# Optimization experiments

Measured on AMD Instinct MI355X. Metric: run time of the kernel, lower is better.

Reference implementation:

```python
import jax, jax.numpy as jnp
import numpy as np

B, S, D = 2, 2048, 1024
H, DH = 16, 64  # num_heads, per-head depth (kd//H == vd//H)
NEG = -1e10


def setup_inputs() -> dict:
    key = jax.random.key(0)
    ks = jax.random.split(key, 5)
    scale = 0.02
    return {
        "X": jax.random.normal(ks[0], (B, S, D), dtype=jnp.float32),
        "Wq": jax.random.normal(ks[1], (D, D), dtype=jnp.float32) * scale,
        "Wk": jax.random.normal(ks[2], (D, D), dtype=jnp.float32) * scale,
        "Wv": jax.random.normal(ks[3], (D, D), dtype=jnp.float32) * scale,
        "Wo": jax.random.normal(ks[4], (D, D), dtype=jnp.float32) * scale,
    }


def reference(X, Wq, Wk, Wv, Wo):
    # torch nn.Linear(in,out,bias=False): y = x @ W.T, W is [out,in]
    q = X @ Wq.T  # [B,S,H*DH]
    k = X @ Wk.T
    v = X @ Wv.T
    # split heads -> [B,H,S,DH]
    q = q.reshape(B, S, H, DH).transpose(0, 2, 1, 3) * (DH ** -0.5)
    k = k.reshape(B, S, H, DH).transpose(0, 2, 1, 3)
    v = v.reshape(B, S, H, DH).transpose(0, 2, 1, 3)
    # causal bias: -1e10 on strictly upper triangle (psuedolikelihood=False)
    bias = NEG * jnp.triu(jnp.ones((S, S), dtype=jnp.float32), 1)
    # logits[...,q,k] = q . k
    logits = jnp.einsum("bhkd,bhqd->bhqk", k, q) + bias
    weights = jax.nn.softmax(logits, axis=-1)  # [B,H,S,S]
    out = jnp.einsum("bhqk,bhkd->bhqd", weights, v)
    out = out.transpose(0, 2, 1, 3).reshape(B, S, H * DH)
    return out @ Wo.T  # [B,S,D]
```

## Files before the change

### kernel.cpp

```cpp
#include <hip/hip_runtime.h>
#include <math.h>


typedef _Float16 f16x8 __attribute__((ext_vector_type(8)));
typedef _Float16 f16x4 __attribute__((ext_vector_type(4)));
typedef _Float16 f16x2 __attribute__((ext_vector_type(2)));
typedef __attribute__((ext_vector_type(4))) float f32x4;
typedef __attribute__((ext_vector_type(16))) float f32x16;

#define MFMA16(a, b, c) __builtin_amdgcn_mfma_f32_16x16x32_f16(a, b, c, 0, 0, 0)
#define MFMA32(a, b, c) __builtin_amdgcn_mfma_f32_32x32x16_f16(a, b, c, 0, 0, 0)
#define QSCALE 0.18033688f

__device__ __forceinline__ void async16(const void* g, void* l) {
  __builtin_amdgcn_global_load_lds(
      (const __attribute__((address_space(1))) unsigned int*)g,
      (__attribute__((address_space(3))) unsigned int*)l, 16, 0, 0);
}

__device__ __forceinline__ f16x2 pk2(float x, float y) {
  return __builtin_bit_cast(f16x2, __builtin_amdgcn_cvt_pkrtz(x, y));
}

__device__ __forceinline__ f16x8 cvt8(const float* __restrict__ p) {
  float4 a = *(const float4*)p;
  float4 b = *(const float4*)(p + 4);
  f16x2 p0 = pk2(a.x, a.y), p1 = pk2(a.z, a.w);
  f16x2 p2 = pk2(b.x, b.y), p3 = pk2(b.z, b.w);
  f16x8 h;
  h[0] = p0[0]; h[1] = p0[1]; h[2] = p1[0]; h[3] = p1[1];
  h[4] = p2[0]; h[5] = p2[1]; h[6] = p3[0]; h[7] = p3[1];
  return h;
}

__global__ void convert_all(const float* __restrict__ X, const float* __restrict__ Wq,
                            const float* __restrict__ Wk, const float* __restrict__ Wv,
                            const float* __restrict__ Wo, _Float16* __restrict__ Xh,
                            _Float16* __restrict__ Wqkvh, _Float16* __restrict__ Woh) {
  size_t i = ((size_t)blockIdx.x * 256 + threadIdx.x) * 8;
  const float* src; _Float16* dst; size_t off;
  if (i < 4194304u)      { src = X;  dst = Xh;              off = i; }
  else if (i < 5242880u) { src = Wq; dst = Wqkvh;           off = i - 4194304u; }
  else if (i < 6291456u) { src = Wk; dst = Wqkvh + 1048576; off = i - 5242880u; }
  else if (i < 7340032u) { src = Wv; dst = Wqkvh + 2097152; off = i - 6291456u; }
  else                   { src = Wo; dst = Woh;             off = i - 7340032u; }
  *(f16x8*)(dst + off) = cvt8(src + off);
}

__global__ __launch_bounds__(256) void gemm_qkv_a(
    const _Float16* __restrict__ Xh, const _Float16* __restrict__ Wh,
    _Float16* __restrict__ Qh, _Float16* __restrict__ Kh,
    _Float16* __restrict__ Vth) {
  __shared__ _Float16 As[128 * 32];
  __shared__ _Float16 Bs[128 * 32];
  const int tid = threadIdx.x;
  const int wave = tid >> 6, lane = tid & 63;
  const int quad = lane >> 4, l16 = lane & 15;
  const int wm = (wave >> 1) * 64, wn = (wave & 1) * 64;
  const int bn = blockIdx.x, bm = blockIdx.y;
  const int mat = bn >> 3;

  const int r0 = tid >> 2, cc0 = (tid & 3) * 8;
  const int r1 = (tid + 256) >> 2, cc1 = (tid & 3) * 8;
  const _Float16* gA0 = &Xh[(size_t)(bm * 128 + r0) * 1024 + cc0];
  const _Float16* gA1 = &Xh[(size_t)(bm * 128 + r1) * 1024 + cc1];
  const _Float16* gB0 = &Wh[(size_t)(bn * 128 + r0) * 1024 + cc0];
  const _Float16* gB1 = &Wh[(size_t)(bn * 128 + r1) * 1024 + cc1];

  f32x4 acc[4][4] = {};

  for (int k0 = 0; k0 < 1024; k0 += 32) {
    __syncthreads();
    async16(gA0 + k0, &As[(wave * 64) * 8]);
    async16(gA1 + k0, &As[(256 + wave * 64) * 8]);
    async16(gB0 + k0, &Bs[(wave * 64) * 8]);
    async16(gB1 + k0, &Bs[(256 + wave * 64) * 8]);
    __syncthreads();
    f16x8 af[4], bf[4];
#pragma unroll
    for (int t = 0; t < 4; ++t) {
      af[t] = *(const f16x8*)&As[(wm + t * 16 + l16) * 32 + quad * 8];
      bf[t] = *(const f16x8*)&Bs[(wn + t * 16 + l16) * 32 + quad * 8];
    }
#pragma unroll
    for (int mt = 0; mt < 4; ++mt)
#pragma unroll
      for (int nt = 0; nt < 4; ++nt)
        acc[mt][nt] = MFMA16(af[mt], bf[nt], acc[mt][nt]);
  }

#pragma unroll
  for (int mt = 0; mt < 4; ++mt) {
    int m_base = bm * 128 + wm + mt * 16 + quad * 4;
    int b = m_base >> 11, sb = m_base & 2047;
#pragma unroll
    for (int nt = 0; nt < 4; ++nt) {
      int ob = (bn * 128 + wn + nt * 16) & 1023;
      int h = ob >> 6;
      int dh = (ob & 63) + l16;
      size_t bh = (size_t)(b * 16 + h);
      if (mat == 0) {
#pragma unroll
        for (int r = 0; r < 4; ++r)
          Qh[(bh * 2048 + sb + r) * 64 + dh] = (_Float16)(acc[mt][nt][r] * QSCALE);
      } else if (mat == 1) {
#pragma unroll
        for (int r = 0; r < 4; ++r)
          Kh[(bh * 2048 + sb + r) * 64 + dh] = (_Float16)acc[mt][nt][r];
      } else {
        f16x4 pk;
        pk[0] = (_Float16)acc[mt][nt][0];
        pk[1] = (_Float16)acc[mt][nt][1];
        pk[2] = (_Float16)acc[mt][nt][2];
        pk[3] = (_Float16)acc[mt][nt][3];
        *(f16x4*)&Vth[(bh * 64 + dh) * 2048 + sb] = pk;
      }
    }
  }
}

__global__ __launch_bounds__(256) void gemm_qkv_f(
    const _Float16* __restrict__ Xh, const float* __restrict__ Wq,
    const float* __restrict__ Wk, const float* __restrict__ Wv,
    _Float16* __restrict__ Qh, _Float16* __restrict__ Kh,
    _Float16* __restrict__ Vth) {
  __shared__ _Float16 As[128 * 72];
  __shared__ _Float16 Bs[128 * 72];
  const int tid = threadIdx.x;
  const int wave = tid >> 6, lane = tid & 63;
  const int quad = lane >> 4, l16 = lane & 15;
  const int wm = (wave >> 1) * 64, wn = (wave & 1) * 64;
  const int bn = blockIdx.x, bm = blockIdx.y;
  const int mat = bn >> 3;
  const float* Bsrc = (mat == 0) ? Wq : (mat == 1) ? Wk : Wv;
  const int brow0 = (bn & 7) * 128;

  f32x4 acc[4][4] = {};

  for (int k0 = 0; k0 < 1024; k0 += 64) {
    __syncthreads();
#pragma unroll
    for (int j = 0; j < 4; ++j) {
      int idx = tid + j * 256;
      int row = idx >> 3, c8 = idx & 7;
      *(int4*)&As[row * 72 + c8 * 8] =
          *(const int4*)&Xh[(size_t)(bm * 128 + row) * 1024 + k0 + c8 * 8];
      *(f16x8*)&Bs[row * 72 + c8 * 8] =
          cvt8(&Bsrc[(size_t)(brow0 + row) * 1024 + k0 + c8 * 8]);
    }
    __syncthreads();
#pragma unroll
    for (int kc = 0; kc < 2; ++kc) {
      f16x8 af[4], bf[4];
#pragma unroll
      for (int t = 0; t < 4; ++t) {
        af[t] = *(const f16x8*)&As[(wm + t * 16 + l16) * 72 + kc * 32 + quad * 8];
        bf[t] = *(const f16x8*)&Bs[(wn + t * 16 + l16) * 72 + kc * 32 + quad * 8];
      }
#pragma unroll
      for (int mt = 0; mt < 4; ++mt)
#pragma unroll
        for (int nt = 0; nt < 4; ++nt)
          acc[mt][nt] = MFMA16(af[mt], bf[nt], acc[mt][nt]);
    }
  }

#pragma unroll
  for (int mt = 0; mt < 4; ++mt) {
    int m_base = bm * 128 + wm + mt * 16 + quad * 4;
    int b = m_base >> 11, sb = m_base & 2047;
#pragma unroll
    for (int nt = 0; nt < 4; ++nt) {
      int ob = (bn * 128 + wn + nt * 16) & 1023;
      int h = ob >> 6;
      int dh = (ob & 63) + l16;
      size_t bh = (size_t)(b * 16 + h);
      if (mat == 0) {
#pragma unroll
        for (int r = 0; r < 4; ++r)
          Qh[(bh * 2048 + sb + r) * 64 + dh] = (_Float16)(acc[mt][nt][r] * QSCALE);
      } else if (mat == 1) {
#pragma unroll
        for (int r = 0; r < 4; ++r)
          Kh[(bh * 2048 + sb + r) * 64 + dh] = (_Float16)acc[mt][nt][r];
      } else {
        f16x4 pk;
        pk[0] = (_Float16)acc[mt][nt][0];
        pk[1] = (_Float16)acc[mt][nt][1];
        pk[2] = (_Float16)acc[mt][nt][2];
        pk[3] = (_Float16)acc[mt][nt][3];
        *(f16x4*)&Vth[(bh * 64 + dh) * 2048 + sb] = pk;
      }
    }
  }
}

__global__ __launch_bounds__(512) void attn_kernel(
    const _Float16* __restrict__ Qg, const _Float16* __restrict__ Kg,
    const _Float16* __restrict__ Vtg, _Float16* __restrict__ Og) {
  __shared__ _Float16 smem[2 * (128 * 72 + 64 * 136)];
  const int bh = blockIdx.x;
  const int qt = 15 - (int)blockIdx.y;
  const int q0 = qt * 128;
  const int tid = threadIdx.x;
  const int group = tid >> 8;
  const int tidg = tid & 255;
  const int wv = (tid >> 6) & 3;
  const int lane = tid & 63;
  const int l31 = lane & 31, hl = lane >> 5;
  const int b = bh >> 4, h = bh & 15;
  const int qrow = q0 + wv * 32 + l31;

  _Float16* Kl = smem + group * (128 * 72 + 64 * 136);
  _Float16* Vl = Kl + 128 * 72;

  const _Float16* Qbase = Qg + ((size_t)bh * 2048 + qrow) * 64 + hl * 8;
  f16x8 aq[4];
#pragma unroll
  for (int t = 0; t < 4; ++t) aq[t] = *(const f16x8*)(Qbase + 16 * t);

  f32x16 oacc[2] = {};
  float la = 0.f, lb = 0.f;

  const int krow = tidg >> 3, kc8 = (tidg & 7) * 8;
  const int vrow = tidg >> 4, vc16 = (tidg & 15) * 8;
  const _Float16* gK = Kg + ((size_t)bh * 2048 + krow) * 64 + kc8;
  const _Float16* gV = Vtg + ((size_t)bh * 64 + vrow) * 2048 + vc16;

  int4 ka0, ka1, ka2, ka3, va0, va1, va2, va3;
  {
    const int ktp = (group <= qt) ? group : qt;
    const _Float16* kp = gK + (size_t)ktp * (128 * 64);
    const _Float16* vp = gV + (size_t)ktp * 128;
    ka0 = *(const int4*)(kp + 0 * 32 * 64);
    ka1 = *(const int4*)(kp + 1 * 32 * 64);
    ka2 = *(const int4*)(kp + 2 * 32 * 64);
    ka3 = *(const int4*)(kp + 3 * 32 * 64);
    va0 = *(const int4*)(vp + 0 * 16 * 2048);
    va1 = *(const int4*)(vp + 1 * 16 * 2048);
    va2 = *(const int4*)(vp + 2 * 16 * 2048);
    va3 = *(const int4*)(vp + 3 * 16 * 2048);
  }

  const int nmax = (qt + 2) >> 1;
  for (int it = 0; it < nmax; ++it) {
    const int kt = 2 * it + group;
    const bool valid = (kt <= qt);
    const int k0 = kt << 7;
    __syncthreads();
    *(int4*)&Kl[(krow + 0) * 72 + kc8] = ka0;
    *(int4*)&Kl[(krow + 32) * 72 + kc8] = ka1;
    *(int4*)&Kl[(krow + 64) * 72 + kc8] = ka2;
    *(int4*)&Kl[(krow + 96) * 72 + kc8] = ka3;
    *(int4*)&Vl[(vrow + 0) * 136 + vc16] = va0;
    *(int4*)&Vl[(vrow + 16) * 136 + vc16] = va1;
    *(int4*)&Vl[(vrow + 32) * 136 + vc16] = va2;
    *(int4*)&Vl[(vrow + 48) * 136 + vc16] = va3;
    {
      const int ktn = (kt + 2 <= qt) ? (kt + 2) : qt;
      const _Float16* kp = gK + (size_t)ktn * (128 * 64);
      const _Float16* vp = gV + (size_t)ktn * 128;
      ka0 = *(const int4*)(kp + 0 * 32 * 64);
      ka1 = *(const int4*)(kp + 1 * 32 * 64);
      ka2 = *(const int4*)(kp + 2 * 32 * 64);
      ka3 = *(const int4*)(kp + 3 * 32 * 64);
      va0 = *(const int4*)(vp + 0 * 16 * 2048);
      va1 = *(const int4*)(vp + 1 * 16 * 2048);
      va2 = *(const int4*)(vp + 2 * 16 * 2048);
      va3 = *(const int4*)(vp + 3 * 16 * 2048);
    }
    __syncthreads();
    if (!valid) continue;

    const bool diag = (kt == qt);

#pragma unroll
    for (int s32t = 0; s32t < 4; ++s32t) {
      f32x16 tv = {};
      __builtin_amdgcn_s_setprio(1);
#pragma unroll
      for (int t = 0; t < 4; ++t) {
        f16x8 kb = *(const f16x8*)&Kl[(s32t * 32 + l31) * 72 + t * 16 + hl * 8];
        tv = MFMA32(kb, aq[t], tv);
      }
      __builtin_amdgcn_s_setprio(0);
      int pkx[8];
#pragma unroll
      for (int i = 0; i < 8; ++i) {
        float x0 = tv[2 * i], x1 = tv[2 * i + 1];
        int kg = k0 + s32t * 32 + ((2 * i) & 3) + 8 * (i >> 1) + 4 * hl;
        if (diag) {
          if (kg > qrow) x0 = -1e30f;
          if (kg + 1 > qrow) x1 = -1e30f;
        }
        x0 = __builtin_amdgcn_exp2f(x0);
        x1 = __builtin_amdgcn_exp2f(x1);
        la += x0;
        lb += x1;
        pkx[i] = __builtin_bit_cast(int, pk2(x0, x1));
      }
      int s0 = hl ? pkx[0] : pkx[2];
      int s1 = hl ? pkx[1] : pkx[3];
      int s2 = hl ? pkx[4] : pkx[6];
      int s3 = hl ? pkx[5] : pkx[7];
      int r0 = __shfl_xor(s0, 32);
      int r1 = __shfl_xor(s1, 32);
      int r2 = __shfl_xor(s2, 32);
      int r3 = __shfl_xor(s3, 32);
      int4 f0, f1;
      f0.x = hl ? r0 : pkx[0];
      f0.y = hl ? r1 : pkx[1];
      f0.z = hl ? pkx[2] : r0;
      f0.w = hl ? pkx[3] : r1;
      f1.x = hl ? r2 : pkx[4];
      f1.y = hl ? r3 : pkx[5];
      f1.z = hl ? pkx[6] : r2;
      f1.w = hl ? pkx[7] : r3;
      f16x8 bp0 = __builtin_bit_cast(f16x8, f0);
      f16x8 bp1 = __builtin_bit_cast(f16x8, f1);
      __builtin_amdgcn_s_setprio(1);
#pragma unroll
      for (int d = 0; d < 2; ++d) {
        f16x8 vb0 = *(const f16x8*)&Vl[(d * 32 + l31) * 136 + s32t * 32 + hl * 8];
        f16x8 vb1 =
            *(const f16x8*)&Vl[(d * 32 + l31) * 136 + s32t * 32 + 16 + hl * 8];
        oacc[d] = MFMA32(vb0, bp0, oacc[d]);
        oacc[d] = MFMA32(vb1, bp1, oacc[d]);
      }
      __builtin_amdgcn_s_setprio(0);
    }
  }

  float lsum = la + lb;
  __syncthreads();
  float* mbuf = (float*)(smem + (128 * 72 + 64 * 136));
  float* slot = mbuf + (wv * 64 + lane) * 33;
  if (group == 1) {
#pragma unroll
    for (int d = 0; d < 2; ++d)
#pragma unroll
      for (int j = 0; j < 16; ++j) slot[d * 16 + j] = oacc[d][j];
    slot[32] = lsum;
  }
  __syncthreads();
  if (group == 0) {
#pragma unroll
    for (int d = 0; d < 2; ++d)
#pragma unroll
      for (int j = 0; j < 16; ++j) oacc[d][j] += slot[d * 16 + j];
    lsum += slot[32];
    lsum += __shfl_xor(lsum, 32);
    float inv = 1.0f / lsum;
#pragma unroll
    for (int d = 0; d < 2; ++d)
#pragma unroll
      for (int rq = 0; rq < 4; ++rq) {
        f16x4 o;
#pragma unroll
        for (int j = 0; j < 4; ++j)
          o[j] = (_Float16)(oacc[d][rq * 4 + j] * inv);
        int dh = d * 32 + 8 * rq + 4 * hl;
        *(f16x4*)&Og[(((size_t)b * 2048 + qrow) * 16 + h) * 64 + dh] = o;
      }
  }
}

__global__ __launch_bounds__(256) void gemm_out_a(
    const _Float16* __restrict__ A, const _Float16* __restrict__ Woh,
    float* __restrict__ Co) {
  __shared__ _Float16 As[128 * 32];
  __shared__ _Float16 Bs[64 * 32];
  const int tid = threadIdx.x;
  const int wave = tid >> 6, lane = tid & 63;
  const int quad = lane >> 4, l16 = lane & 15;
  const int wm = (wave >> 1) * 64, wn = (wave & 1) * 32;
  const int bn = blockIdx.x, bm = blockIdx.y;

  const int r0 = tid >> 2, cc0 = (tid & 3) * 8;
  const int r1 = (tid + 256) >> 2;
  const _Float16* gA0 = &A[(size_t)(bm * 128 + r0) * 1024 + cc0];
  const _Float16* gA1 = &A[(size_t)(bm * 128 + r1) * 1024 + cc0];
  const _Float16* gB0 = &Woh[(size_t)(bn * 64 + r0) * 1024 + cc0];

  f32x4 acc[4][2] = {};

  for (int k0 = 0; k0 < 1024; k0 += 32) {
    __syncthreads();
    async16(gA0 + k0, &As[(wave * 64) * 8]);
    async16(gA1 + k0, &As[(256 + wave * 64) * 8]);
    if (r0 < 64) async16(gB0 + k0, &Bs[(wave * 64) * 8]);
    __syncthreads();
    f16x8 af[4], bf[2];
#pragma unroll
    for (int t = 0; t < 4; ++t)
      af[t] = *(const f16x8*)&As[(wm + t * 16 + l16) * 32 + quad * 8];
#pragma unroll
    for (int t = 0; t < 2; ++t)
      bf[t] = *(const f16x8*)&Bs[(wn + t * 16 + l16) * 32 + quad * 8];
#pragma unroll
    for (int mt = 0; mt < 4; ++mt)
#pragma unroll
      for (int nt = 0; nt < 2; ++nt)
        acc[mt][nt] = MFMA16(af[mt], bf[nt], acc[mt][nt]);
  }

#pragma unroll
  for (int mt = 0; mt < 4; ++mt) {
    int m_base = bm * 128 + wm + mt * 16 + quad * 4;
#pragma unroll
    for (int nt = 0; nt < 2; ++nt) {
      int n = bn * 64 + wn + nt * 16 + l16;
#pragma unroll
      for (int r = 0; r < 4; ++r)
        Co[(size_t)(m_base + r) * 1024 + n] = acc[mt][nt][r];
    }
  }
}

__global__ __launch_bounds__(256) void gemm_out_f(
    const _Float16* __restrict__ A, const float* __restrict__ Wo,
    float* __restrict__ Co) {
  __shared__ _Float16 As[128 * 72];
  __shared__ _Float16 Bs[64 * 72];
  const int tid = threadIdx.x;
  const int wave = tid >> 6, lane = tid & 63;
  const int quad = lane >> 4, l16 = lane & 15;
  const int wm = (wave >> 1) * 64, wn = (wave & 1) * 32;
  const int bn = blockIdx.x, bm = blockIdx.y;

  f32x4 acc[4][2] = {};

  for (int k0 = 0; k0 < 1024; k0 += 64) {
    __syncthreads();
#pragma unroll
    for (int j = 0; j < 4; ++j) {
      int idx = tid + j * 256;
      int row = idx >> 3, c8 = idx & 7;
      *(int4*)&As[row * 72 + c8 * 8] =
          *(const int4*)&A[(size_t)(bm * 128 + row) * 1024 + k0 + c8 * 8];
    }
#pragma unroll
    for (int j = 0; j < 2; ++j) {
      int idx = tid + j * 256;
      int row = idx >> 3, c8 = idx & 7;
      *(f16x8*)&Bs[row * 72 + c8 * 8] =
          cvt8(&Wo[(size_t)(bn * 64 + row) * 1024 + k0 + c8 * 8]);
    }
    __syncthreads();
#pragma unroll
    for (int kc = 0; kc < 2; ++kc) {
      f16x8 af[4], bf[2];
#pragma unroll
      for (int t = 0; t < 4; ++t)
        af[t] = *(const f16x8*)&As[(wm + t * 16 + l16) * 72 + kc * 32 + quad * 8];
#pragma unroll
      for (int t = 0; t < 2; ++t)
        bf[t] = *(const f16x8*)&Bs[(wn + t * 16 + l16) * 72 + kc * 32 + quad * 8];
#pragma unroll
      for (int mt = 0; mt < 4; ++mt)
#pragma unroll
        for (int nt = 0; nt < 2; ++nt)
          acc[mt][nt] = MFMA16(af[mt], bf[nt], acc[mt][nt]);
    }
  }

#pragma unroll
  for (int mt = 0; mt < 4; ++mt) {
    int m_base = bm * 128 + wm + mt * 16 + quad * 4;
#pragma unroll
    for (int nt = 0; nt < 2; ++nt) {
      int n = bn * 64 + wn + nt * 16 + l16;
#pragma unroll
      for (int r = 0; r < 4; ++r)
        Co[(size_t)(m_base + r) * 1024 + n] = acc[mt][nt][r];
    }
  }
}

extern "C" void kernel_launch(void* const* d_in, const int* in_sizes, int n_in,
                              void* d_out, int out_size, void* d_ws, size_t ws_size,
                              hipStream_t stream) {
  const float* X  = (const float*)d_in[0];
  const float* Wq = (const float*)d_in[1];
  const float* Wk = (const float*)d_in[2];
  const float* Wv = (const float*)d_in[3];
  const float* Wo = (const float*)d_in[4];
  float* out = (float*)d_out;

  _Float16* Qh    = (_Float16*)d_out;
  _Float16* Kh    = Qh + 4194304;
  _Float16* Vth   = (_Float16*)d_ws;
  _Float16* Xh    = Vth + 4194304;
  _Float16* Og    = Xh;
  _Float16* Wqkvh = Xh + 4194304;
  _Float16* Woh   = Wqkvh + 3145728;

  const bool big = (ws_size >= 25165824u);

  convert_all<<<big ? 4096 : 2048, 256, 0, stream>>>(X, Wq, Wk, Wv, Wo,
                                                     Xh, Wqkvh, Woh);
  if (big)
    gemm_qkv_a<<<dim3(24, 32), 256, 0, stream>>>(Xh, Wqkvh, Qh, Kh, Vth);
  else
    gemm_qkv_f<<<dim3(24, 32), 256, 0, stream>>>(Xh, Wq, Wk, Wv, Qh, Kh, Vth);
  attn_kernel<<<dim3(32, 16), 512, 0, stream>>>(Qh, Kh, Vth, Og);
  if (big)
    gemm_out_a<<<dim3(16, 32), 256, 0, stream>>>(Og, Woh, out);
  else
    gemm_out_f<<<dim3(16, 32), 256, 0, stream>>>(Og, Wo, out);
}
```

Before: 175.7 us.

## Drop LDS staging in attention; read K/V directly from global, skip masked diagonal subtiles

The attention kernel no longer stages K and V tiles through shared memory with a two-group split over key tiles. Each 256-thread block now walks all key tiles itself, loading MFMA operands straight from global memory or cache. On the diagonal tile each wave skips the 32-key subtiles that lie fully above its query rows. This removes the barriers, LDS writes and cross-group reduction, but every wave now reads K/V separately from global memory with strided accesses, and per-block parallelism is halved.

After: 231.3 us. 1.32x slower.

```diff
diff --git a/kernel.cpp b/kernel.cpp
--- a/kernel.cpp
+++ b/kernel.cpp
@@ -195,92 +195,42 @@
   }
 }
 
-__global__ __launch_bounds__(512) void attn_kernel(
+__global__ __launch_bounds__(256) void attn_kernel(
     const _Float16* __restrict__ Qg, const _Float16* __restrict__ Kg,
     const _Float16* __restrict__ Vtg, _Float16* __restrict__ Og) {
-  __shared__ _Float16 smem[2 * (128 * 72 + 64 * 136)];
   const int bh = blockIdx.x;
   const int qt = 15 - (int)blockIdx.y;
   const int q0 = qt * 128;
   const int tid = threadIdx.x;
-  const int group = tid >> 8;
-  const int tidg = tid & 255;
-  const int wv = (tid >> 6) & 3;
+  const int wv = tid >> 6;
   const int lane = tid & 63;
   const int l31 = lane & 31, hl = lane >> 5;
   const int b = bh >> 4, h = bh & 15;
   const int qrow = q0 + wv * 32 + l31;
 
-  _Float16* Kl = smem + group * (128 * 72 + 64 * 136);
-  _Float16* Vl = Kl + 128 * 72;
-
   const _Float16* Qbase = Qg + ((size_t)bh * 2048 + qrow) * 64 + hl * 8;
   f16x8 aq[4];
 #pragma unroll
   for (int t = 0; t < 4; ++t) aq[t] = *(const f16x8*)(Qbase + 16 * t);
 
+  const _Float16* Kb = Kg + (size_t)bh * 2048 * 64;
+  const _Float16* Vb = Vtg + (size_t)bh * 64 * 2048;
+
   f32x16 oacc[2] = {};
   float la = 0.f, lb = 0.f;
 
-  const int krow = tidg >> 3, kc8 = (tidg & 7) * 8;
-  const int vrow = tidg >> 4, vc16 = (tidg & 15) * 8;
-  const _Float16* gK = Kg + ((size_t)bh * 2048 + krow) * 64 + kc8;
-  const _Float16* gV = Vtg + ((size_t)bh * 64 + vrow) * 2048 + vc16;
-
-  int4 ka0, ka1, ka2, ka3, va0, va1, va2, va3;
-  {
-    const int ktp = (group <= qt) ? group : qt;
-    const _Float16* kp = gK + (size_t)ktp * (128 * 64);
-    const _Float16* vp = gV + (size_t)ktp * 128;
-    ka0 = *(const int4*)(kp + 0 * 32 * 64);
-    ka1 = *(const int4*)(kp + 1 * 32 * 64);
-    ka2 = *(const int4*)(kp + 2 * 32 * 64);
-    ka3 = *(const int4*)(kp + 3 * 32 * 64);
-    va0 = *(const int4*)(vp + 0 * 16 * 2048);
-    va1 = *(const int4*)(vp + 1 * 16 * 2048);
-    va2 = *(const int4*)(vp + 2 * 16 * 2048);
-    va3 = *(const int4*)(vp + 3 * 16 * 2048);
-  }
-
-  const int nmax = (qt + 2) >> 1;
-  for (int it = 0; it < nmax; ++it) {
-    const int kt = 2 * it + group;
-    const bool valid = (kt <= qt);
+  for (int kt = 0; kt <= qt; ++kt) {
     const int k0 = kt << 7;
-    __syncthreads();
-    *(int4*)&Kl[(krow + 0) * 72 + kc8] = ka0;
-    *(int4*)&Kl[(krow + 32) * 72 + kc8] = ka1;
-    *(int4*)&Kl[(krow + 64) * 72 + kc8] = ka2;
-    *(int4*)&Kl[(krow + 96) * 72 + kc8] = ka3;
-    *(int4*)&Vl[(vrow + 0) * 136 + vc16] = va0;
-    *(int4*)&Vl[(vrow + 16) * 136 + vc16] = va1;
-    *(int4*)&Vl[(vrow + 32) * 136 + vc16] = va2;
-    *(int4*)&Vl[(vrow + 48) * 136 + vc16] = va3;
-    {
-      const int ktn = (kt + 2 <= qt) ? (kt + 2) : qt;
-      const _Float16* kp = gK + (size_t)ktn * (128 * 64);
-      const _Float16* vp = gV + (size_t)ktn * 128;
-      ka0 = *(const int4*)(kp + 0 * 32 * 64);
-      ka1 = *(const int4*)(kp + 1 * 32 * 64);
-      ka2 = *(const int4*)(kp + 2 * 32 * 64);
-      ka3 = *(const int4*)(kp + 3 * 32 * 64);
-      va0 = *(const int4*)(vp + 0 * 16 * 2048);
-      va1 = *(const int4*)(vp + 1 * 16 * 2048);
-      va2 = *(const int4*)(vp + 2 * 16 * 2048);
-      va3 = *(const int4*)(vp + 3 * 16 * 2048);
-    }
-    __syncthreads();
-    if (!valid) continue;
-
     const bool diag = (kt == qt);
-
-#pragma unroll
-    for (int s32t = 0; s32t < 4; ++s32t) {
+    const int smax = diag ? (wv + 1) : 4;
+
+    for (int s32t = 0; s32t < smax; ++s32t) {
       f32x16 tv = {};
       __builtin_amdgcn_s_setprio(1);
 #pragma unroll
       for (int t = 0; t < 4; ++t) {
-        f16x8 kb = *(const f16x8*)&Kl[(s32t * 32 + l31) * 72 + t * 16 + hl * 8];
+        f16x8 kb =
+            *(const f16x8*)&Kb[(size_t)(k0 + s32t * 32 + l31) * 64 + t * 16 + hl * 8];
         tv = MFMA32(kb, aq[t], tv);
       }
       __builtin_amdgcn_s_setprio(0);
@@ -321,9 +271,10 @@
       __builtin_amdgcn_s_setprio(1);
 #pragma unroll
       for (int d = 0; d < 2; ++d) {
-        f16x8 vb0 = *(const f16x8*)&Vl[(d * 32 + l31) * 136 + s32t * 32 + hl * 8];
+        f16x8 vb0 =
+            *(const f16x8*)&Vb[(size_t)(d * 32 + l31) * 2048 + k0 + s32t * 32 + hl * 8];
         f16x8 vb1 =
-            *(const f16x8*)&Vl[(d * 32 + l31) * 136 + s32t * 32 + 16 + hl * 8];
+            *(const f16x8*)&Vb[(size_t)(d * 32 + l31) * 2048 + k0 + s32t * 32 + 16 + hl * 8];
         oacc[d] = MFMA32(vb0, bp0, oacc[d]);
         oacc[d] = MFMA32(vb1, bp1, oacc[d]);
       }
@@ -332,37 +283,19 @@
   }
 
   float lsum = la + lb;
-  __syncthreads();
-  float* mbuf = (float*)(smem + (128 * 72 + 64 * 136));
-  float* slot = mbuf + (wv * 64 + lane) * 33;
-  if (group == 1) {
-#pragma unroll
-    for (int d = 0; d < 2; ++d)
-#pragma unroll
-      for (int j = 0; j < 16; ++j) slot[d * 16 + j] = oacc[d][j];
-    slot[32] = lsum;
-  }
-  __syncthreads();
-  if (group == 0) {
-#pragma unroll
-    for (int d = 0; d < 2; ++d)
-#pragma unroll
-      for (int j = 0; j < 16; ++j) oacc[d][j] += slot[d * 16 + j];
-    lsum += slot[32];
-    lsum += __shfl_xor(lsum, 32);
-    float inv = 1.0f / lsum;
-#pragma unroll
-    for (int d = 0; d < 2; ++d)
-#pragma unroll
-      for (int rq = 0; rq < 4; ++rq) {
-        f16x4 o;
-#pragma unroll
-        for (int j = 0; j < 4; ++j)
-          o[j] = (_Float16)(oacc[d][rq * 4 + j] * inv);
-        int dh = d * 32 + 8 * rq + 4 * hl;
-        *(f16x4*)&Og[(((size_t)b * 2048 + qrow) * 16 + h) * 64 + dh] = o;
-      }
-  }
+  lsum += __shfl_xor(lsum, 32);
+  float inv = 1.0f / lsum;
+#pragma unroll
+  for (int d = 0; d < 2; ++d)
+#pragma unroll
+    for (int rq = 0; rq < 4; ++rq) {
+      f16x4 o;
+#pragma unroll
+      for (int j = 0; j < 4; ++j)
+        o[j] = (_Float16)(oacc[d][rq * 4 + j] * inv);
+      int dh = d * 32 + 8 * rq + 4 * hl;
+      *(f16x4*)&Og[(((size_t)b * 2048 + qrow) * 16 + h) * 64 + dh] = o;
+    }
 }
 
 __global__ __launch_bounds__(256) void gemm_out_a(
@@ -503,7 +436,7 @@
     gemm_qkv_a<<<dim3(24, 32), 256, 0, stream>>>(Xh, Wqkvh, Qh, Kh, Vth);
   else
     gemm_qkv_f<<<dim3(24, 32), 256, 0, stream>>>(Xh, Wq, Wk, Wv, Qh, Kh, Vth);
-  attn_kernel<<<dim3(32, 16), 512, 0, stream>>>(Qh, Kh, Vth, Og);
+  attn_kernel<<<dim3(32, 16), 256, 0, stream>>>(Qh, Kh, Vth, Og);
   if (big)
     gemm_out_a<<<dim3(16, 32), 256, 0, stream>>>(Og, Woh, out);
   else
```
